# Performance work log

Measured on AMD Instinct MI355X. Metric: run time of the kernel, lower is better.

The kernel has to match this reference:

```python
import jax, jax.numpy as jnp
import numpy as np

N = 50000      # nodes
E = 800000     # edges
IN = 128       # in_dim
OUT = 128      # out_dim
R = 4          # num_relations
H = 8          # heads
D = OUT // H   # per-head dim
NEG_SLOPE = 0.2


def setup_inputs() -> dict:
    key = jax.random.key(0)
    ks = jax.random.split(key, 12)
    s = 0.05
    return {
        "node_inp": jax.random.normal(ks[0], (N, IN), dtype=jnp.float32),
        "edge_index": jax.random.randint(ks[1], (2, E), 0, N),
        "edge_type": jax.random.randint(ks[2], (E,), 0, R),
        # per-relation GATConv params
        "W_rel": jax.random.normal(ks[3], (R, IN, OUT), dtype=jnp.float32) * s,
        "att_src_rel": jax.random.normal(ks[4], (R, H, D), dtype=jnp.float32) * s,
        "att_dst_rel": jax.random.normal(ks[5], (R, H, D), dtype=jnp.float32) * s,
        "bias_rel": jax.random.normal(ks[6], (R, OUT), dtype=jnp.float32) * s,
        # linear layers
        "W_self": jax.random.normal(ks[7], (IN, OUT), dtype=jnp.float32) * s,   # lin_self
        "W_cross": jax.random.normal(ks[8], (OUT, OUT), dtype=jnp.float32) * s,  # lin_cross
        # lang_conv GAT params (lin_l is Bypass, so no weight matrix)
        "att_src_lang": jax.random.normal(ks[9], (H, D), dtype=jnp.float32) * s,
        "att_dst_lang": jax.random.normal(ks[10], (H, D), dtype=jnp.float32) * s,
        "bias_lang": jax.random.normal(ks[11], (OUT,), dtype=jnp.float32) * s,
    }


def _hgnn_forward(node_inp, edge_index, edge_type, W_rel, att_src_rel,
                  att_dst_rel, bias_rel, W_self, W_cross,
                  att_src_lang, att_dst_lang, bias_lang):
    src, dst = edge_index[0], edge_index[1]

    def rel_gat(W, a_s, a_d, b, mask):
        # standard PyG GATConv (single x, add_self_loops=False), restricted to
        # edges with this relation type via mask
        x = (node_inp @ W).reshape(N, H, D)                     # [N,H,D]
        es = jnp.einsum('nhd,hd->nh', x, a_s)
        ed = jnp.einsum('nhd,hd->nh', x, a_d)
        logit = jax.nn.leaky_relu(es[src] + ed[dst], NEG_SLOPE)  # [E,H]
        logit = jnp.where(mask[:, None], logit, -1e30)
        mx = jax.ops.segment_max(logit, dst, num_segments=N)     # [N,H]
        mx = jnp.maximum(mx, -1e30)                              # avoid -inf
        p = jnp.exp(logit - mx[dst]) * mask[:, None]
        den = jax.ops.segment_sum(p, dst, num_segments=N)        # [N,H]
        alpha = p / jnp.where(den > 0, den, 1.0)[dst]            # [E,H]
        msg = alpha[..., None] * x[src]                          # [E,H,D]
        out = jax.ops.segment_sum(msg, dst, num_segments=N)      # [N,H,D]
        tmask = jax.ops.segment_sum(mask.astype(jnp.float32), dst,
                                    num_segments=N) > 0          # [N] target nodes
        return out.reshape(N, OUT) + b, tmask

    rel_masks = edge_type[None, :] == jnp.arange(R)[:, None]     # [R,E]
    rel_out, tmask = jax.vmap(rel_gat)(W_rel, att_src_rel, att_dst_rel,
                                       bias_rel, rel_masks)      # [R,N,OUT],[R,N]
    h = jax.nn.gelu(rel_out, approximate=False) @ W_cross        # [R,N,OUT]

    S = node_inp @ W_self                                        # [N,OUT] self entries
    # lang_conv: per node i, GAT attention over entries {self(i)} U
    # {rel outputs at i for relations where i is a target}. lin_l = Bypass,
    # and since x is a single tensor in PyG, x_dst = rel_inputs[i] = S[i].
    ent = jnp.concatenate([S[None], h], axis=0).reshape(R + 1, N, H, D)
    valid = jnp.concatenate([jnp.ones((1, N), bool), tmask], axis=0)  # [R+1,N]
    ls = jnp.einsum('knhd,hd->knh', ent, att_src_lang)
    ld = jnp.einsum('nhd,hd->nh', ent[0], att_dst_lang)
    logit = jax.nn.leaky_relu(ls + ld[None], NEG_SLOPE)          # [R+1,N,H]
    logit = jnp.where(valid[..., None], logit, -jnp.inf)
    alpha = jax.nn.softmax(logit, axis=0)                        # self always valid
    out = jnp.einsum('knh,knhd->nhd', alpha, ent).reshape(N, OUT)
    return out + bias_lang


def reference(node_inp, edge_index, edge_type, W_rel, att_src_rel, att_dst_rel,
              bias_rel, W_self, W_cross, att_src_lang, att_dst_lang, bias_lang):
    return _hgnn_forward(node_inp, edge_index, edge_type, W_rel, att_src_rel,
                         att_dst_rel, bias_rel, W_self, W_cross,
                         att_src_lang, att_dst_lang, bias_lang)
```

## Files before the change

### kernel.cpp

```cpp
#include <hip/hip_runtime.h>
#include <hip/hip_bf16.h>
#include <math.h>

#define NN 50000
#define NE 800000
#define NREL 4
#define NHEAD 8
#define NSEG (NREL * NN)
#define BCAP 22

typedef __hip_bfloat16 bf16;
typedef short short8 __attribute__((ext_vector_type(8)));
typedef float floatx4 __attribute__((ext_vector_type(4)));

#define LOG2E 1.4426950408889634f

__device__ __forceinline__ float b2f(bf16 v) { return __bfloat162float(v); }
__device__ __forceinline__ float us2f(unsigned short u) {
    return __uint_as_float(((unsigned)u) << 16);
}
__device__ __forceinline__ unsigned short f2us(float v) {
    bf16 b = __float2bfloat16(v);
    return *(unsigned short*)&b;
}

__device__ __forceinline__ float gelu_f(float v) {
    float z = v * 0.70710678118654752f;
    float az = fabsf(z);
    float t = __builtin_amdgcn_rcpf(__builtin_fmaf(0.3275911f, az, 1.f));
    float p = t * (0.254829592f +
              t * (-0.284496736f +
              t * (1.421413741f +
              t * (-1.453152027f +
              t * 1.061405429f))));
    float ex = __builtin_amdgcn_exp2f(az * az * -LOG2E);
    float er = copysignf(1.f - p * ex, z);
    return 0.5f * v * (1.f + er);
}

__global__ void fill_kernel(float* __restrict__ out, int n) {
    int t = blockIdx.x * blockDim.x + threadIdx.x;
    if (t < n) out[t] = 1000.0f;
}

__global__ __launch_bounds__(256) void prep_scatter(
    const float* __restrict__ W_rel,
    const float* __restrict__ W_self,
    const float* __restrict__ W_cross,
    const float* __restrict__ a_src,
    const float* __restrict__ a_dst,
    const float* __restrict__ a_src_lang,
    const float* __restrict__ a_dst_lang,
    const float* __restrict__ node_inp,
    const int* __restrict__ ei,
    const int* __restrict__ et,
    bf16* __restrict__ Wt, bf16* __restrict__ Wct,
    bf16* __restrict__ Ab,
    int* __restrict__ counts,
    unsigned short* __restrict__ bkt) {
    int t = blockIdx.x * blockDim.x + threadIdx.x;

    int src = 0, pos = BCAP;
    unsigned seg = 0;
    if (t < NE) {
        src = ei[t];
        int dst = ei[NE + t];
        seg = (unsigned)(et[t] * NN + dst);
        pos = atomicAdd(&counts[seg], 1);
    }

    if (t < 768 * 128) {
        int row = t >> 7, k = t & 127;
        float v;
        if (row < 512) {
            int r = row >> 7, c = row & 127;
            v = W_rel[(r * 128 + k) * 128 + c];
        } else if (row < 640) {
            v = W_self[k * 128 + (row - 512)];
        } else if (row < 704) {
            int q = row - 640;
            bool is_src = q < 32;
            int qq = is_src ? q : q - 32;
            int r = qq >> 3, h = qq & 7;
            const float* av = (is_src ? a_src : a_dst) + (r * 8 + h) * 16;
            const float* wr = W_rel + (size_t)(r * 128 + k) * 128 + h * 16;
            float s = 0.f;
            #pragma unroll
            for (int dd = 0; dd < 16; ++dd) s += wr[dd] * av[dd];
            v = s * LOG2E;
        } else if (row < 720) {
            int q2 = row - 704;
            bool is_ts = q2 < 8;
            int h = q2 & 7;
            const float* av = (is_ts ? a_src_lang : a_dst_lang) + h * 16;
            const float* wr = W_self + k * 128 + h * 16;
            float s = 0.f;
            #pragma unroll
            for (int dd = 0; dd < 16; ++dd) s += wr[dd] * av[dd];
            v = s * LOG2E;
        } else {
            v = 0.f;
        }
        Wt[t] = __float2bfloat16(v);
    } else if (t < 768 * 128 + 144 * 128) {
        int u = t - 768 * 128;
        int n = u >> 7, k = u & 127;
        float v;
        if (n < 128) {
            v = W_cross[k * 128 + n];
        } else {
            int h = n - 128;
            if (h < 8) {
                const float* av = a_src_lang + h * 16;
                const float* wr = W_cross + k * 128 + h * 16;
                float s = 0.f;
                #pragma unroll
                for (int dd = 0; dd < 16; ++dd) s += wr[dd] * av[dd];
                v = s * LOG2E;
            } else {
                v = 0.f;
            }
        }
        Wct[u] = __float2bfloat16(v);
    }

    if (t < NN * 16) {
        const float* ap = node_inp + (size_t)t * 8;
        float4 f0 = *(const float4*)ap;
        float4 f1 = *(const float4*)(ap + 4);
        short8 v = (short8){(short)f2us(f0.x), (short)f2us(f0.y),
                            (short)f2us(f0.z), (short)f2us(f0.w),
                            (short)f2us(f1.x), (short)f2us(f1.y),
                            (short)f2us(f1.z), (short)f2us(f1.w)};
        *(short8*)(Ab + (size_t)t * 8) = v;
    }

    if (t < NE && pos < BCAP)
        bkt[seg * (unsigned)BCAP + (unsigned)pos] = (unsigned short)src;
}

__global__ __launch_bounds__(256) void gemm_node(
    const bf16* __restrict__ Ab,
    const bf16* __restrict__ Bt,
    bf16* __restrict__ outb,
    float* __restrict__ outf,
    unsigned short* __restrict__ es_u,
    unsigned short* __restrict__ ed_u,
    unsigned short* __restrict__ tsd,
    int M)
{
    __shared__ __align__(16) char smem[25600];
    short (*As)[40] = (short (*)[40])smem;
    short (*Bs)[40] = (short (*)[40])(smem + 5120);

    const int tid  = threadIdx.x;
    const int wave = tid >> 6, lane = tid & 63;
    const int quad = lane >> 4, l16 = lane & 15;
    const int wr_ = wave & 1, wc = wave >> 1;
    const int row0 = blockIdx.x * 64;
    const int plane = blockIdx.y;
    const int col0 = plane * 256;

    floatx4 acc[2][8];
    #pragma unroll
    for (int i = 0; i < 2; ++i)
        #pragma unroll
        for (int j = 0; j < 8; ++j) acc[i][j] = (floatx4){0.f, 0.f, 0.f, 0.f};

    for (int k0 = 0; k0 < 128; k0 += 32) {
        {
            int c = tid;
            int r = c >> 2, off = (c & 3) * 8;
            int gr = row0 + r;
            short8 v = {0, 0, 0, 0, 0, 0, 0, 0};
            if (gr < M)
                v = *(const short8*)(Ab + (((size_t)gr) << 7) + k0 + off);
            *(short8*)&As[r][off] = v;
        }
        #pragma unroll
        for (int i = 0; i < 4; ++i) {
            int c = i * 256 + tid;
            int r = c >> 2, off = (c & 3) * 8;
            short8 w = *(const short8*)(Bt + (((size_t)(col0 + r)) << 7) + k0 + off);
            *(short8*)&Bs[r][off] = w;
        }
        __syncthreads();

        short8 av[2], bv[8];
        #pragma unroll
        for (int mt = 0; mt < 2; ++mt)
            av[mt] = *(const short8*)&As[wr_ * 32 + mt * 16 + l16][quad * 8];
        #pragma unroll
        for (int nt = 0; nt < 8; ++nt)
            bv[nt] = *(const short8*)&Bs[wc * 128 + nt * 16 + l16][quad * 8];
        #pragma unroll
        for (int mt = 0; mt < 2; ++mt)
            #pragma unroll
            for (int nt = 0; nt < 8; ++nt)
                acc[mt][nt] = __builtin_amdgcn_mfma_f32_16x16x32_bf16(
                    av[mt], bv[nt], acc[mt][nt], 0, 0, 0);
        __syncthreads();
    }

    if (plane == 2 && wc == 1) {
        #pragma unroll
        for (int mt = 0; mt < 2; ++mt) {
            #pragma unroll
            for (int reg = 0; reg < 4; ++reg) {
                int gr = row0 + wr_ * 32 + mt * 16 + quad * 4 + reg;
                if (gr >= M) continue;
                #pragma unroll
                for (int nt = 0; nt < 5; ++nt) {
                    int q = nt * 16 + l16;
                    unsigned short v = f2us(acc[mt][nt][reg]);
                    if (q < 32)
                        es_u[(unsigned)((q >> 3) * NN + gr) * 8u + (unsigned)(q & 7)] = v;
                    else if (q < 64)
                        ed_u[(unsigned)(((q - 32) >> 3) * NN + gr) * 8u + (unsigned)((q - 32) & 7)] = v;
                    else
                        tsd[(unsigned)gr * 16u + (unsigned)(q - 64)] = v;
                }
            }
        }
        return;
    }

    float* ct = (float*)(smem + wave * 4352);
    const int rr2 = lane >> 2;
    const int cc0 = (lane & 3) * 16;
    const int gr2base = row0 + wr_ * 32 + rr2;

    for (int mt = 0; mt < 2; ++mt) {
        #pragma unroll
        for (int half = 0; half < 2; ++half) {
            #pragma unroll
            for (int nt = 0; nt < 4; ++nt)
                #pragma unroll
                for (int reg = 0; reg < 4; ++reg)
                    ct[(quad * 4 + reg) * 68 + nt * 16 + l16] =
                        acc[mt][half * 4 + nt][reg];
            int gr2 = gr2base + mt * 16;
            if (gr2 < M) {
                float4 f0 = *(const float4*)&ct[rr2 * 68 + cc0];
                float4 f1 = *(const float4*)&ct[rr2 * 68 + cc0 + 4];
                float4 f2 = *(const float4*)&ct[rr2 * 68 + cc0 + 8];
                float4 f3 = *(const float4*)&ct[rr2 * 68 + cc0 + 12];
                int lc = half * 64 + cc0;
                if (plane == 2) {
                    float* dst = outf + (((size_t)gr2) << 7) + lc;
                    __builtin_nontemporal_store(*(const floatx4*)&f0, (floatx4*)dst);
                    __builtin_nontemporal_store(*(const floatx4*)&f1, (floatx4*)(dst + 4));
                    __builtin_nontemporal_store(*(const floatx4*)&f2, (floatx4*)(dst + 8));
                    __builtin_nontemporal_store(*(const floatx4*)&f3, (floatx4*)(dst + 12));
                } else {
                    int rel = plane * 2 + wc;
                    float tmp[16] = {f0.x, f0.y, f0.z, f0.w, f1.x, f1.y, f1.z, f1.w,
                                     f2.x, f2.y, f2.z, f2.w, f3.x, f3.y, f3.z, f3.w};
                    short8 o0, o1;
                    #pragma unroll
                    for (int j = 0; j < 8; ++j) o0[j] = (short)f2us(tmp[j]);
                    #pragma unroll
                    for (int j = 0; j < 8; ++j) o1[j] = (short)f2us(tmp[8 + j]);
                    bf16* dst = outb + ((size_t)(rel * NN + gr2) << 7) + lc;
                    *(short8*)dst = o0;
                    *(short8*)(dst + 8) = o1;
                }
            }
        }
    }
}

__global__ __launch_bounds__(256) void agg_kernel(
    const unsigned short* __restrict__ bkt, const int* __restrict__ counts,
    const bf16* __restrict__ Xb, const unsigned short* __restrict__ es_u,
    const unsigned short* __restrict__ ed_u, const float* __restrict__ bias_rel,
    bf16* __restrict__ Gb4, unsigned char* __restrict__ flag)
{
    const int rel  = blockIdx.y;
    const int wave = threadIdx.x >> 6, l = threadIdx.x & 63;
    const int n    = blockIdx.x * 16 + wave * 4 + (l >> 4);
    const int l16  = l & 15;
    const int f0   = l16 * 8;
    const int h    = l16 >> 1;

    const unsigned seg = (unsigned)(rel * NN + n);
    int cnt = counts[seg];
    cnt = cnt < BCAP ? cnt : BCAP;
    const unsigned short* bk  = bkt + seg * (unsigned)BCAP;
    const float edv = us2f(ed_u[seg * 8u + (unsigned)h]);
    const unsigned short* Xr  = (const unsigned short*)Xb +
                                (size_t)rel * (size_t)(NN * 128);
    const unsigned short* esr = es_u + (unsigned)rel * (unsigned)(NN * 8);

    float a[8];
    #pragma unroll
    for (int j = 0; j < 8; ++j) a[j] = 0.f;
    float den = 0.f;

    int e = 0;
    for (; e + 1 < cnt; e += 2) {
        unsigned pair = *(const unsigned*)(bk + e);
        int s0 = (int)(pair & 0xFFFFu);
        int s1 = (int)(pair >> 16);
        float e0 = us2f(esr[(unsigned)s0 * 8u + (unsigned)h]);
        float e1 = us2f(esr[(unsigned)s1 * 8u + (unsigned)h]);
        short8 u0 = *(const short8*)(Xr + (size_t)s0 * 128 + f0);
        short8 u1 = *(const short8*)(Xr + (size_t)s1 * 128 + f0);
        float aa0 = e0 + edv, aa1 = e1 + edv;
        float w0 = __builtin_amdgcn_exp2f(fmaxf(aa0, 0.2f * aa0));
        float w1 = __builtin_amdgcn_exp2f(fmaxf(aa1, 0.2f * aa1));
        #pragma unroll
        for (int j = 0; j < 8; ++j)
            a[j] += w0 * us2f((unsigned short)u0[j]) +
                    w1 * us2f((unsigned short)u1[j]);
        den += w0 + w1;
    }
    if (e < cnt) {
        int s0 = (int)bk[e];
        float e0 = us2f(esr[(unsigned)s0 * 8u + (unsigned)h]);
        short8 u0 = *(const short8*)(Xr + (size_t)s0 * 128 + f0);
        float aa0 = e0 + edv;
        float w0 = __builtin_amdgcn_exp2f(fmaxf(aa0, 0.2f * aa0));
        #pragma unroll
        for (int j = 0; j < 8; ++j) a[j] += w0 * us2f((unsigned short)u0[j]);
        den += w0;
    }

    float inv = den > 0.f ? __builtin_amdgcn_rcpf(den) : 0.f;
    const float* bp = bias_rel + rel * 128 + f0;
    float4 b0 = *(const float4*)bp;
    float4 b1 = *(const float4*)(bp + 4);
    float bb[8] = {b0.x, b0.y, b0.z, b0.w, b1.x, b1.y, b1.z, b1.w};
    short8 o;
    #pragma unroll
    for (int j = 0; j < 8; ++j)
        o[j] = (short)f2us(gelu_f(__builtin_fmaf(a[j], inv, bb[j])));
    __builtin_nontemporal_store(o, (short8*)((unsigned short*)Gb4 +
        ((size_t)((unsigned)n * 4u + (unsigned)rel)) * 128u + (unsigned)f0));
    if (l16 == 0)
        flag[(unsigned)n * 4u + (unsigned)rel] = (unsigned char)(cnt > 0);
}

__global__ __launch_bounds__(256) void gemm_lang(
    const bf16* __restrict__ A,
    const bf16* __restrict__ Bt,
    const unsigned char* __restrict__ flag,
    const unsigned short* __restrict__ tsd,
    const float* __restrict__ bias_lang,
    float* __restrict__ out)
{
    __shared__ __align__(16) char smem[16640];
    short (*As)[40] = (short (*)[40])smem;
    short (*Bs)[40] = (short (*)[40])(smem + 5120);
    float (*ls_lds)[4][9] = (float (*)[4][9])smem;

    const int M = NN * NREL;
    const int tid  = threadIdx.x;
    const int wave = tid >> 6, lane = tid & 63;
    const int quad = lane >> 4, l16 = lane & 15;
    const int wr_ = wave & 1, wc = wave >> 1;
    const int row0 = blockIdx.x * 64;
    const int node0 = blockIdx.x * 16;

    float svp[2][4];
    unsigned flw[2];
    float tsv[2][4], tdv[2][4];
    #pragma unroll
    for (int mt = 0; mt < 2; ++mt) {
        int node = node0 + wr_ * 8 + mt * 4 + quad;
        flw[mt] = *(const unsigned*)(flag + (unsigned)node * 4u);
        #pragma unroll
        for (int nt = 0; nt < 4; ++nt) {
            int hh = wc * 4 + nt;
            svp[mt][nt] = out[(unsigned)node * 128u + (unsigned)(wc * 64 + nt * 16 + l16)];
            tsv[mt][nt] = us2f(tsd[(unsigned)node * 16u + (unsigned)hh]);
            tdv[mt][nt] = us2f(tsd[(unsigned)node * 16u + 8u + (unsigned)hh]);
        }
    }

    floatx4 acc[2][4];
    floatx4 accl[2];
    #pragma unroll
    for (int i = 0; i < 2; ++i) {
        #pragma unroll
        for (int j = 0; j < 4; ++j) acc[i][j] = (floatx4){0.f, 0.f, 0.f, 0.f};
        accl[i] = (floatx4){0.f, 0.f, 0.f, 0.f};
    }

    for (int k0 = 0; k0 < 128; k0 += 32) {
        {
            int c = tid;
            int r = c >> 2, off = (c & 3) * 8;
            int gr = row0 + r;
            short8 v = {0, 0, 0, 0, 0, 0, 0, 0};
            if (gr < M)
                v = *(const short8*)(A + (((size_t)gr) << 7) + k0 + off);
            *(short8*)&As[r][off] = v;
        }
        #pragma unroll
        for (int i = 0; i < 3; ++i) {
            int c = i * 256 + tid;
            if (c < 576) {
                int r = c >> 2, off = (c & 3) * 8;
                short8 w = *(const short8*)(Bt + (((size_t)r) << 7) + k0 + off);
                *(short8*)&Bs[r][off] = w;
            }
        }
        __syncthreads();

        short8 av[2], bv[4], bvl;
        #pragma unroll
        for (int mt = 0; mt < 2; ++mt)
            av[mt] = *(const short8*)&As[wr_ * 32 + mt * 16 + l16][quad * 8];
        #pragma unroll
        for (int nt = 0; nt < 4; ++nt)
            bv[nt] = *(const short8*)&Bs[wc * 64 + nt * 16 + l16][quad * 8];
        bvl = *(const short8*)&Bs[wc * 64 + 64 + l16][quad * 8];
        #pragma unroll
        for (int mt = 0; mt < 2; ++mt) {
            #pragma unroll
            for (int nt = 0; nt < 4; ++nt)
                acc[mt][nt] = __builtin_amdgcn_mfma_f32_16x16x32_bf16(
                    av[mt], bv[nt], acc[mt][nt], 0, 0, 0);
            if (wc)
                accl[mt] = __builtin_amdgcn_mfma_f32_16x16x32_bf16(
                    av[mt], bvl, accl[mt], 0, 0, 0);
        }
        __syncthreads();
    }

    if (wc == 1 && l16 < 8) {
        #pragma unroll
        for (int mt = 0; mt < 2; ++mt) {
            int nl = wr_ * 8 + mt * 4 + quad;
            #pragma unroll
            for (int reg = 0; reg < 4; ++reg)
                ls_lds[nl][reg][l16] = accl[mt][reg];
        }
    }
    __syncthreads();

    #pragma unroll
    for (int nt = 0; nt < 4; ++nt) {
        int col = wc * 64 + nt * 16 + l16;
        float bl = bias_lang[col];
        int hh = wc * 4 + nt;
        #pragma unroll
        for (int mt = 0; mt < 2; ++mt) {
            int nl = wr_ * 8 + mt * 4 + quad;
            int node = node0 + nl;
            float Sv = svp[mt][nt];
            float ts = tsv[mt][nt];
            float td = tdv[mt][nt];
            float g0 = ls_lds[nl][0][hh] + td;
            float g1 = ls_lds[nl][1][hh] + td;
            float g2 = ls_lds[nl][2][hh] + td;
            float g3 = ls_lds[nl][3][hh] + td;
            float aS = ts + td;
            float lS = fmaxf(aS, 0.2f * aS);
            float l0 = fmaxf(g0, 0.2f * g0);
            float l1 = fmaxf(g1, 0.2f * g1);
            float l2 = fmaxf(g2, 0.2f * g2);
            float l3 = fmaxf(g3, 0.2f * g3);
            unsigned fl = flw[mt];
            bool v0 = (fl & 0x000000FFu) != 0, v1 = (fl & 0x0000FF00u) != 0;
            bool v2 = (fl & 0x00FF0000u) != 0, v3 = (fl & 0xFF000000u) != 0;
            float m = lS;
            if (v0) m = fmaxf(m, l0);
            if (v1) m = fmaxf(m, l1);
            if (v2) m = fmaxf(m, l2);
            if (v3) m = fmaxf(m, l3);
            float eS = __builtin_amdgcn_exp2f(lS - m);
            float e0 = v0 ? __builtin_amdgcn_exp2f(l0 - m) : 0.f;
            float e1 = v1 ? __builtin_amdgcn_exp2f(l1 - m) : 0.f;
            float e2 = v2 ? __builtin_amdgcn_exp2f(l2 - m) : 0.f;
            float e3 = v3 ? __builtin_amdgcn_exp2f(l3 - m) : 0.f;
            float sum = eS + e0 + e1 + e2 + e3;
            float o = eS * Sv + e0 * acc[mt][nt][0] + e1 * acc[mt][nt][1] +
                      e2 * acc[mt][nt][2] + e3 * acc[mt][nt][3];
            o = o / sum + bl;
            __builtin_nontemporal_store(o, &out[(unsigned)node * 128u + (unsigned)col]);
        }
    }
}

extern "C" void kernel_launch(void* const* d_in, const int* in_sizes, int n_in,
                              void* d_out, int out_size, void* d_ws, size_t ws_size,
                              hipStream_t stream) {
    const float* node_inp     = (const float*)d_in[0];
    const int*   edge_index   = (const int*)d_in[1];
    const int*   edge_type    = (const int*)d_in[2];
    const float* W_rel        = (const float*)d_in[3];
    const float* att_src_rel  = (const float*)d_in[4];
    const float* att_dst_rel  = (const float*)d_in[5];
    const float* bias_rel     = (const float*)d_in[6];
    const float* W_self       = (const float*)d_in[7];
    const float* W_cross      = (const float*)d_in[8];
    const float* att_src_lang = (const float*)d_in[9];
    const float* att_dst_lang = (const float*)d_in[10];
    const float* bias_lang    = (const float*)d_in[11];
    (void)in_sizes; (void)n_in;

    const size_t SZ_XB   = (size_t)NREL * NN * 128 * 2;
    const size_t SZ_ES   = (size_t)NREL * NN * 8 * 2;
    const size_t SZ_TSD  = (size_t)NN * 16 * 2;
    const size_t SZ_GB4  = (size_t)NREL * NN * 128 * 2;
    const size_t SZ_WT   = 768 * 128 * 2;
    const size_t SZ_WCT  = 144 * 128 * 2;
    const size_t SZ_BKT  = (size_t)NSEG * BCAP * 2;
    const size_t SZ_CNT  = (size_t)NSEG * 4;
    const size_t SZ_FLG  = (size_t)NN * 4;
    const size_t TOTAL = SZ_XB + 2 * SZ_ES + SZ_TSD + SZ_GB4 + SZ_WT + SZ_WCT +
                         SZ_BKT + SZ_CNT + SZ_FLG;

    if (ws_size < TOTAL) {
        fill_kernel<<<(out_size + 255) / 256, 256, 0, stream>>>((float*)d_out, out_size);
        return;
    }

    char* ws = (char*)d_ws;
    size_t o = 0;
    bf16*  Xb      = (bf16*)(ws + o);  o += SZ_XB;
    unsigned short* es_u = (unsigned short*)(ws + o); o += SZ_ES;
    unsigned short* ed_u = (unsigned short*)(ws + o); o += SZ_ES;
    unsigned short* tsd  = (unsigned short*)(ws + o); o += SZ_TSD;
    bf16*  Gb4     = (bf16*)(ws + o);  o += SZ_GB4;
    bf16*  Wt      = (bf16*)(ws + o);  o += SZ_WT;
    bf16*  Wct     = (bf16*)(ws + o);  o += SZ_WCT;
    unsigned short* bkt = (unsigned short*)(ws + o); o += SZ_BKT;
    int*   counts  = (int*)(ws + o);   o += SZ_CNT;
    unsigned char* flag = (unsigned char*)(ws + o);
    float* S       = (float*)d_out;
    bf16*  Ab      = Gb4;

    hipMemsetAsync(counts, 0, SZ_CNT, stream);

    prep_scatter<<<(NE + 255) / 256, 256, 0, stream>>>(
        W_rel, W_self, W_cross, att_src_rel, att_dst_rel, att_src_lang,
        att_dst_lang, node_inp, edge_index, edge_type, Wt, Wct, Ab, counts, bkt);

    dim3 g1((NN + 63) / 64, 3);
    gemm_node<<<g1, 256, 0, stream>>>(Ab, Wt, Xb, S, es_u, ed_u, tsd, NN);

    dim3 ga(NN / 16, NREL);
    agg_kernel<<<ga, 256, 0, stream>>>(bkt, counts, Xb, es_u, ed_u, bias_rel, Gb4, flag);

    dim3 g2((NREL * NN + 63) / 64, 1);
    gemm_lang<<<g2, 256, 0, stream>>>(Gb4, Wct, flag, tsd, bias_lang, (float*)d_out);
}
```

Before: 265.6 us.

## Recompute self projection inside gemm_lang instead of storing fp32 S

Plane 2 of gemm_node previously computed the self projection S and wrote it as fp32 into the output buffer, and gemm_lang read it back. Now gemm_node's plane 2 computes only the attention-score columns, with a narrower tile. gemm_lang reloads node_inp, converts it to bf16 and computes S on the fly with extra MFMAs, reading the W_self rows directly from global memory. This removes the fp32 write and read of S at the cost of reading node_inp again and doing some redundant conversion and compute in gemm_lang.

Result: slower. 280.2 us (+5.5%).

```diff
diff --git a/kernel.cpp b/kernel.cpp
--- a/kernel.cpp
+++ b/kernel.cpp
@@ -143,7 +143,6 @@
     const bf16* __restrict__ Ab,
     const bf16* __restrict__ Bt,
     bf16* __restrict__ outb,
-    float* __restrict__ outf,
     unsigned short* __restrict__ es_u,
     unsigned short* __restrict__ ed_u,
     unsigned short* __restrict__ tsd,
@@ -159,101 +158,72 @@
     const int wr_ = wave & 1, wc = wave >> 1;
     const int row0 = blockIdx.x * 64;
     const int plane = blockIdx.y;
-    const int col0 = plane * 256;
-
-    floatx4 acc[2][8];
-    #pragma unroll
-    for (int i = 0; i < 2; ++i)
-        #pragma unroll
-        for (int j = 0; j < 8; ++j) acc[i][j] = (floatx4){0.f, 0.f, 0.f, 0.f};
-
-    for (int k0 = 0; k0 < 128; k0 += 32) {
-        {
-            int c = tid;
-            int r = c >> 2, off = (c & 3) * 8;
-            int gr = row0 + r;
-            short8 v = {0, 0, 0, 0, 0, 0, 0, 0};
-            if (gr < M)
-                v = *(const short8*)(Ab + (((size_t)gr) << 7) + k0 + off);
-            *(short8*)&As[r][off] = v;
-        }
-        #pragma unroll
-        for (int i = 0; i < 4; ++i) {
-            int c = i * 256 + tid;
-            int r = c >> 2, off = (c & 3) * 8;
-            short8 w = *(const short8*)(Bt + (((size_t)(col0 + r)) << 7) + k0 + off);
-            *(short8*)&Bs[r][off] = w;
-        }
-        __syncthreads();
-
-        short8 av[2], bv[8];
-        #pragma unroll
-        for (int mt = 0; mt < 2; ++mt)
-            av[mt] = *(const short8*)&As[wr_ * 32 + mt * 16 + l16][quad * 8];
-        #pragma unroll
-        for (int nt = 0; nt < 8; ++nt)
-            bv[nt] = *(const short8*)&Bs[wc * 128 + nt * 16 + l16][quad * 8];
-        #pragma unroll
-        for (int mt = 0; mt < 2; ++mt)
+
+    if (plane < 2) {
+        const int col0 = plane * 256;
+        floatx4 acc[2][8];
+        #pragma unroll
+        for (int i = 0; i < 2; ++i)
+            #pragma unroll
+            for (int j = 0; j < 8; ++j) acc[i][j] = (floatx4){0.f, 0.f, 0.f, 0.f};
+
+        for (int k0 = 0; k0 < 128; k0 += 32) {
+            {
+                int c = tid;
+                int r = c >> 2, off = (c & 3) * 8;
+                int gr = row0 + r;
+                short8 v = {0, 0, 0, 0, 0, 0, 0, 0};
+                if (gr < M)
+                    v = *(const short8*)(Ab + (((size_t)gr) << 7) + k0 + off);
+                *(short8*)&As[r][off] = v;
+            }
+            #pragma unroll
+            for (int i = 0; i < 4; ++i) {
+                int c = i * 256 + tid;
+                int r = c >> 2, off = (c & 3) * 8;
+                short8 w = *(const short8*)(Bt + (((size_t)(col0 + r)) << 7) + k0 + off);
+                *(short8*)&Bs[r][off] = w;
+            }
+            __syncthreads();
+
+            short8 av[2], bv[8];
+            #pragma unroll
+            for (int mt = 0; mt < 2; ++mt)
+                av[mt] = *(const short8*)&As[wr_ * 32 + mt * 16 + l16][quad * 8];
             #pragma unroll
             for (int nt = 0; nt < 8; ++nt)
-                acc[mt][nt] = __builtin_amdgcn_mfma_f32_16x16x32_bf16(
-                    av[mt], bv[nt], acc[mt][nt], 0, 0, 0);
-        __syncthreads();
-    }
-
-    if (plane == 2 && wc == 1) {
-        #pragma unroll
+                bv[nt] = *(const short8*)&Bs[wc * 128 + nt * 16 + l16][quad * 8];
+            #pragma unroll
+            for (int mt = 0; mt < 2; ++mt)
+                #pragma unroll
+                for (int nt = 0; nt < 8; ++nt)
+                    acc[mt][nt] = __builtin_amdgcn_mfma_f32_16x16x32_bf16(
+                        av[mt], bv[nt], acc[mt][nt], 0, 0, 0);
+            __syncthreads();
+        }
+
+        float* ct = (float*)(smem + wave * 4352);
+        const int rr2 = lane >> 2;
+        const int cc0 = (lane & 3) * 16;
+        const int gr2base = row0 + wr_ * 32 + rr2;
+        const int rel = plane * 2 + wc;
+
         for (int mt = 0; mt < 2; ++mt) {
             #pragma unroll
-            for (int reg = 0; reg < 4; ++reg) {
-                int gr = row0 + wr_ * 32 + mt * 16 + quad * 4 + reg;
-                if (gr >= M) continue;
+            for (int half = 0; half < 2; ++half) {
                 #pragma unroll
-                for (int nt = 0; nt < 5; ++nt) {
-                    int q = nt * 16 + l16;
-                    unsigned short v = f2us(acc[mt][nt][reg]);
-                    if (q < 32)
-                        es_u[(unsigned)((q >> 3) * NN + gr) * 8u + (unsigned)(q & 7)] = v;
-                    else if (q < 64)
-                        ed_u[(unsigned)(((q - 32) >> 3) * NN + gr) * 8u + (unsigned)((q - 32) & 7)] = v;
-                    else
-                        tsd[(unsigned)gr * 16u + (unsigned)(q - 64)] = v;
-                }
-            }
-        }
-        return;
-    }
-
-    float* ct = (float*)(smem + wave * 4352);
-    const int rr2 = lane >> 2;
-    const int cc0 = (lane & 3) * 16;
-    const int gr2base = row0 + wr_ * 32 + rr2;
-
-    for (int mt = 0; mt < 2; ++mt) {
-        #pragma unroll
-        for (int half = 0; half < 2; ++half) {
-            #pragma unroll
-            for (int nt = 0; nt < 4; ++nt)
-                #pragma unroll
-                for (int reg = 0; reg < 4; ++reg)
-                    ct[(quad * 4 + reg) * 68 + nt * 16 + l16] =
-                        acc[mt][half * 4 + nt][reg];
-            int gr2 = gr2base + mt * 16;
-            if (gr2 < M) {
-                float4 f0 = *(const float4*)&ct[rr2 * 68 + cc0];
-                float4 f1 = *(const float4*)&ct[rr2 * 68 + cc0 + 4];
-                float4 f2 = *(const float4*)&ct[rr2 * 68 + cc0 + 8];
-                float4 f3 = *(const float4*)&ct[rr2 * 68 + cc0 + 12];
-                int lc = half * 64 + cc0;
-                if (plane == 2) {
-                    float* dst = outf + (((size_t)gr2) << 7) + lc;
-                    __builtin_nontemporal_store(*(const floatx4*)&f0, (floatx4*)dst);
-                    __builtin_nontemporal_store(*(const floatx4*)&f1, (floatx4*)(dst + 4));
-                    __builtin_nontemporal_store(*(const floatx4*)&f2, (floatx4*)(dst + 8));
-                    __builtin_nontemporal_store(*(const floatx4*)&f3, (floatx4*)(dst + 12));
-                } else {
-                    int rel = plane * 2 + wc;
+                for (int nt = 0; nt < 4; ++nt)
+                    #pragma unroll
+                    for (int reg = 0; reg < 4; ++reg)
+                        ct[(quad * 4 + reg) * 68 + nt * 16 + l16] =
+                            acc[mt][half * 4 + nt][reg];
+                int gr2 = gr2base + mt * 16;
+                if (gr2 < M) {
+                    float4 f0 = *(const float4*)&ct[rr2 * 68 + cc0];
+                    float4 f1 = *(const float4*)&ct[rr2 * 68 + cc0 + 4];
+                    float4 f2 = *(const float4*)&ct[rr2 * 68 + cc0 + 8];
+                    float4 f3 = *(const float4*)&ct[rr2 * 68 + cc0 + 12];
+                    int lc = half * 64 + cc0;
                     float tmp[16] = {f0.x, f0.y, f0.z, f0.w, f1.x, f1.y, f1.z, f1.w,
                                      f2.x, f2.y, f2.z, f2.w, f3.x, f3.y, f3.z, f3.w};
                     short8 o0, o1;
@@ -267,6 +237,68 @@
                 }
             }
         }
+        return;
+    }
+
+    floatx4 acc[2][4];
+    #pragma unroll
+    for (int i = 0; i < 2; ++i)
+        #pragma unroll
+        for (int j = 0; j < 4; ++j) acc[i][j] = (floatx4){0.f, 0.f, 0.f, 0.f};
+
+    for (int k0 = 0; k0 < 128; k0 += 32) {
+        {
+            int c = tid;
+            int r = c >> 2, off = (c & 3) * 8;
+            int gr = row0 + r;
+            short8 v = {0, 0, 0, 0, 0, 0, 0, 0};
+            if (gr < M)
+                v = *(const short8*)(Ab + (((size_t)gr) << 7) + k0 + off);
+            *(short8*)&As[r][off] = v;
+        }
+        #pragma unroll
+        for (int i = 0; i < 2; ++i) {
+            int c = i * 256 + tid;
+            int r = c >> 2, off = (c & 3) * 8;
+            short8 w = *(const short8*)(Bt + (((size_t)(640 + r)) << 7) + k0 + off);
+            *(short8*)&Bs[r][off] = w;
+        }
+        __syncthreads();
+
+        short8 av[2], bv[4];
+        #pragma unroll
+        for (int mt = 0; mt < 2; ++mt)
+            av[mt] = *(const short8*)&As[wr_ * 32 + mt * 16 + l16][quad * 8];
+        #pragma unroll
+        for (int nt = 0; nt < 4; ++nt)
+            bv[nt] = *(const short8*)&Bs[wc * 64 + nt * 16 + l16][quad * 8];
+        #pragma unroll
+        for (int mt = 0; mt < 2; ++mt)
+            #pragma unroll
+            for (int nt = 0; nt < 4; ++nt)
+                acc[mt][nt] = __builtin_amdgcn_mfma_f32_16x16x32_bf16(
+                    av[mt], bv[nt], acc[mt][nt], 0, 0, 0);
+        __syncthreads();
+    }
+
+    #pragma unroll
+    for (int mt = 0; mt < 2; ++mt) {
+        #pragma unroll
+        for (int reg = 0; reg < 4; ++reg) {
+            int gr = row0 + wr_ * 32 + mt * 16 + quad * 4 + reg;
+            if (gr >= M) continue;
+            #pragma unroll
+            for (int nt = 0; nt < 4; ++nt) {
+                int q = wc * 64 + nt * 16 + l16;
+                unsigned short v = f2us(acc[mt][nt][reg]);
+                if (q < 32)
+                    es_u[(unsigned)((q >> 3) * NN + gr) * 8u + (unsigned)(q & 7)] = v;
+                else if (q < 64)
+                    ed_u[(unsigned)(((q - 32) >> 3) * NN + gr) * 8u + (unsigned)((q - 32) & 7)] = v;
+                else if (q < 80)
+                    tsd[(unsigned)gr * 16u + (unsigned)(q - 64)] = v;
+            }
+        }
     }
 }
 
@@ -344,14 +376,17 @@
 __global__ __launch_bounds__(256) void gemm_lang(
     const bf16* __restrict__ A,
     const bf16* __restrict__ Bt,
+    const bf16* __restrict__ Wt,
+    const float* __restrict__ node_inp,
     const unsigned char* __restrict__ flag,
     const unsigned short* __restrict__ tsd,
     const float* __restrict__ bias_lang,
     float* __restrict__ out)
 {
-    __shared__ __align__(16) char smem[16640];
+    __shared__ __align__(16) char smem[18944];
     short (*As)[40] = (short (*)[40])smem;
     short (*Bs)[40] = (short (*)[40])(smem + 5120);
+    short (*A2s)[16][36] = (short (*)[16][36])(smem + 16640);
     float (*ls_lds)[4][9] = (float (*)[4][9])smem;
 
     const int M = NN * NREL;
@@ -362,7 +397,6 @@
     const int row0 = blockIdx.x * 64;
     const int node0 = blockIdx.x * 16;
 
-    float svp[2][4];
     unsigned flw[2];
     float tsv[2][4], tdv[2][4];
     #pragma unroll
@@ -372,7 +406,6 @@
         #pragma unroll
         for (int nt = 0; nt < 4; ++nt) {
             int hh = wc * 4 + nt;
-            svp[mt][nt] = out[(unsigned)node * 128u + (unsigned)(wc * 64 + nt * 16 + l16)];
             tsv[mt][nt] = us2f(tsd[(unsigned)node * 16u + (unsigned)hh]);
             tdv[mt][nt] = us2f(tsd[(unsigned)node * 16u + 8u + (unsigned)hh]);
         }
@@ -380,12 +413,15 @@
 
     floatx4 acc[2][4];
     floatx4 accl[2];
+    floatx4 accs[4];
     #pragma unroll
     for (int i = 0; i < 2; ++i) {
         #pragma unroll
         for (int j = 0; j < 4; ++j) acc[i][j] = (floatx4){0.f, 0.f, 0.f, 0.f};
         accl[i] = (floatx4){0.f, 0.f, 0.f, 0.f};
     }
+    #pragma unroll
+    for (int j = 0; j < 4; ++j) accs[j] = (floatx4){0.f, 0.f, 0.f, 0.f};
 
     for (int k0 = 0; k0 < 128; k0 += 32) {
         {
@@ -406,9 +442,21 @@
                 *(short8*)&Bs[r][off] = w;
             }
         }
+        if (tid < 128) {
+            int wr2 = tid >> 6, rr = (tid >> 2) & 15, q = tid & 3;
+            int node = node0 + wr2 * 8 + (rr & 1) * 4 + (rr >> 2);
+            const float* ap = node_inp + (size_t)node * 128 + k0 + q * 8;
+            float4 f0 = *(const float4*)ap;
+            float4 f1 = *(const float4*)(ap + 4);
+            short8 v = (short8){(short)f2us(f0.x), (short)f2us(f0.y),
+                                (short)f2us(f0.z), (short)f2us(f0.w),
+                                (short)f2us(f1.x), (short)f2us(f1.y),
+                                (short)f2us(f1.z), (short)f2us(f1.w)};
+            *(short8*)&A2s[wr2][rr][q * 8] = v;
+        }
         __syncthreads();
 
-        short8 av[2], bv[4], bvl;
+        short8 av[2], bv[4], bvl, av2, bvs[4];
         #pragma unroll
         for (int mt = 0; mt < 2; ++mt)
             av[mt] = *(const short8*)&As[wr_ * 32 + mt * 16 + l16][quad * 8];
@@ -416,6 +464,11 @@
         for (int nt = 0; nt < 4; ++nt)
             bv[nt] = *(const short8*)&Bs[wc * 64 + nt * 16 + l16][quad * 8];
         bvl = *(const short8*)&Bs[wc * 64 + 64 + l16][quad * 8];
+        av2 = *(const short8*)&A2s[wr_][l16][quad * 8];
+        #pragma unroll
+        for (int nt = 0; nt < 4; ++nt)
+            bvs[nt] = *(const short8*)(Wt +
+                (((size_t)(512 + wc * 64 + nt * 16 + l16)) << 7) + k0 + quad * 8);
         #pragma unroll
         for (int mt = 0; mt < 2; ++mt) {
             #pragma unroll
@@ -426,6 +479,10 @@
                 accl[mt] = __builtin_amdgcn_mfma_f32_16x16x32_bf16(
                     av[mt], bvl, accl[mt], 0, 0, 0);
         }
+        #pragma unroll
+        for (int nt = 0; nt < 4; ++nt)
+            accs[nt] = __builtin_amdgcn_mfma_f32_16x16x32_bf16(
+                av2, bvs[nt], accs[nt], 0, 0, 0);
         __syncthreads();
     }
 
@@ -449,7 +506,7 @@
         for (int mt = 0; mt < 2; ++mt) {
             int nl = wr_ * 8 + mt * 4 + quad;
             int node = node0 + nl;
-            float Sv = svp[mt][nt];
+            float Sv = accs[nt][mt];
             float ts = tsv[mt][nt];
             float td = tdv[mt][nt];
             float g0 = ls_lds[nl][0][hh] + td;
@@ -530,7 +587,6 @@
     unsigned short* bkt = (unsigned short*)(ws + o); o += SZ_BKT;
     int*   counts  = (int*)(ws + o);   o += SZ_CNT;
     unsigned char* flag = (unsigned char*)(ws + o);
-    float* S       = (float*)d_out;
     bf16*  Ab      = Gb4;
 
     hipMemsetAsync(counts, 0, SZ_CNT, stream);
@@ -540,11 +596,12 @@
         att_dst_lang, node_inp, edge_index, edge_type, Wt, Wct, Ab, counts, bkt);
 
     dim3 g1((NN + 63) / 64, 3);
-    gemm_node<<<g1, 256, 0, stream>>>(Ab, Wt, Xb, S, es_u, ed_u, tsd, NN);
+    gemm_node<<<g1, 256, 0, stream>>>(Ab, Wt, Xb, es_u, ed_u, tsd, NN);
 
     dim3 ga(NN / 16, NREL);
     agg_kernel<<<ga, 256, 0, stream>>>(bkt, counts, Xb, es_u, ed_u, bias_rel, Gb4, flag);
 
     dim3 g2((NREL * NN + 63) / 64, 1);
-    gemm_lang<<<g2, 256, 0, stream>>>(Gb4, Wct, flag, tsd, bias_lang, (float*)d_out);
-}
+    gemm_lang<<<g2, 256, 0, stream>>>(Gb4, Wct, Wt, node_inp, flag, tsd,
+                                      bias_lang, (float*)d_out);
+}
```
